# Performance work log

Hardware: AMD Instinct MI355X
Metric: run time of the kernel (lower is better)

The kernel has to match this reference:

```python
import jax, jax.numpy as jnp
import numpy as np

D_MODEL = 1024
D_MEMORY = 768
NUM_HEADS = 16
HEAD_DIM = D_MODEL // NUM_HEADS


def _linear_params(key, d_in, d_out):
    kw, kb = jax.random.split(key)
    bound = 1.0 / np.sqrt(d_in)
    W = jax.random.uniform(kw, (d_out, d_in), jnp.float32, -bound, bound)
    b = jax.random.uniform(kb, (d_out,), jnp.float32, -bound, bound)
    return W, b


def setup_inputs() -> dict:
    key = jax.random.key(0)
    ks = jax.random.split(key, 9)
    B, S, M = 2, 2048, 4096
    query = jax.random.normal(ks[0], (B, S, D_MODEL), jnp.float32)
    memory_keys = jax.random.normal(ks[1], (B, M, D_MEMORY), jnp.float32)
    memory_values = jax.random.normal(ks[2], (B, M, D_MEMORY), jnp.float32)
    Wq, bq = _linear_params(ks[3], D_MODEL, D_MODEL)
    Wk, bk = _linear_params(ks[4], D_MEMORY, D_MODEL)
    Wv, bv = _linear_params(ks[5], D_MEMORY, D_MODEL)
    Wo, bo = _linear_params(ks[6], D_MODEL, D_MODEL)
    Wg1, bg1 = _linear_params(ks[7], 2 * D_MODEL, D_MODEL)
    Wg2, bg2 = _linear_params(ks[8], D_MODEL, 1)
    return dict(query=query, memory_keys=memory_keys, memory_values=memory_values,
                Wq=Wq, bq=bq, Wk=Wk, bk=bk, Wv=Wv, bv=bv, Wo=Wo, bo=bo,
                Wg1=Wg1, bg1=bg1, Wg2=Wg2, bg2=bg2)


def reference(query, memory_keys, memory_values,
              Wq, bq, Wk, bk, Wv, bv, Wo, bo, Wg1, bg1, Wg2, bg2):
    B, S, _ = query.shape
    M = memory_keys.shape[1]
    H, Dh = NUM_HEADS, HEAD_DIM
    # projections (torch Linear: x @ W.T + b)
    Q = (query @ Wq.T + bq).reshape(B, S, H, Dh)
    K = (memory_keys @ Wk.T + bk).reshape(B, M, H, Dh)
    V = (memory_values @ Wv.T + bv).reshape(B, M, H, Dh)
    scale = Dh ** -0.5
    attn = jnp.einsum('bshd,bmhd->bhsm', Q, K) * scale
    attn = jax.nn.softmax(attn, axis=-1)
    retrieved = jnp.einsum('bhsm,bmhd->bshd', attn, V).reshape(B, S, H * Dh)
    retrieved = retrieved @ Wo.T + bo
    # gate: Linear -> SiLU -> Linear -> Sigmoid on [query; retrieved]
    g = jnp.concatenate([query, retrieved], axis=-1) @ Wg1.T + bg1
    g = jax.nn.silu(g)
    gate = jax.nn.sigmoid(g @ Wg2.T + bg2)  # [B,S,1]
    return query + gate * retrieved
```

## Files before the change

kernel.cpp:

```cpp
#include <hip/hip_runtime.h>

typedef __attribute__((ext_vector_type(8))) __bf16 bf16x8;
typedef __attribute__((ext_vector_type(4))) float f32x4;
typedef __attribute__((ext_vector_type(8))) unsigned short u16x8;

__device__ __forceinline__ ushort f2bf(float x) {
    unsigned u = __builtin_bit_cast(unsigned, x);
    unsigned r = u + 0x7fffu + ((u >> 16) & 1u);
    return (ushort)(r >> 16);
}
__device__ __forceinline__ float bf2f(ushort u) {
    unsigned v = ((unsigned)u) << 16;
    return __builtin_bit_cast(float, v);
}

__device__ __forceinline__ unsigned cvtpk(float lo, float hi) {
    unsigned r;
    asm("v_cvt_pk_bf16_f32 %0, %1, %2" : "=v"(r) : "v"(lo), "v"(hi));
    return r;
}

__device__ __forceinline__ void gload16(const void* g, void* l) {
    __builtin_amdgcn_global_load_lds(
        (const __attribute__((address_space(1))) void*)g,
        (__attribute__((address_space(3))) void*)l,
        16, 0, 0);
}

__global__ __launch_bounds__(256) void cvt_f32_bf16(const float* __restrict__ in,
                                                    ushort* __restrict__ out, int n4) {
    int i = blockIdx.x * 256 + threadIdx.x;
    int stride = gridDim.x * 256;
    for (; i < n4; i += stride) {
        float4 v = ((const float4*)in)[i];
        ushort4 o;
        o.x = f2bf(v.x); o.y = f2bf(v.y); o.z = f2bf(v.z); o.w = f2bf(v.w);
        ((ushort4*)out)[i] = o;
    }
}

__global__ __launch_bounds__(256) void cvt_query_cat(const float* __restrict__ in,
                                                     ushort* __restrict__ cat) {
    const int r = blockIdx.x, t = threadIdx.x;
    float4 v = ((const float4*)(in + (size_t)r * 1024))[t];
    ushort4 o;
    o.x = f2bf(v.x); o.y = f2bf(v.y); o.z = f2bf(v.z); o.w = f2bf(v.w);
    ((ushort4*)(cat + (size_t)r * 2048))[t] = o;
}

template<int EPI>
__global__ __launch_bounds__(256) void gemm_bt(
    const ushort* __restrict__ A, int lda,
    const ushort* __restrict__ Bw, int ldb,
    const float* __restrict__ bias,
    ushort* __restrict__ o_bf, int ld0,
    float* __restrict__ o_f32,
    int K, float scale)
{
    __shared__ __align__(1024) char smem[49152];
    char* As = smem;
    char* Bs = smem + 32768;
    const int t = threadIdx.x, w = t >> 6, l = t & 63, g = l >> 4, c = l & 15;
    const int wr = w >> 1, wc = w & 1;
    const long m0 = (long)blockIdx.y * 128, n0 = (long)blockIdx.x * 64;
    const size_t ldaB = (size_t)lda * 2, ldbB = (size_t)ldb * 2;
    const int swz = (c & 7) << 4;

    f32x4 acc[4][2];
#pragma unroll
    for (int i = 0; i < 4; ++i)
#pragma unroll
        for (int j = 0; j < 2; ++j) acc[i][j] = (f32x4)0.0f;

    auto stage = [&](int kt, int bufsel) {
        const char* Ab = (const char*)A + (size_t)kt * 128;
        const char* Bb = (const char*)Bw + (size_t)kt * 128;
#pragma unroll
        for (int i = 0; i < 4; ++i) {
            int o = (i * 4 + w) * 1024 + l * 16;
            int row = o >> 7, cb = o & 127;
            gload16(Ab + (size_t)(m0 + row) * ldaB + (cb ^ ((row & 7) << 4)),
                    As + bufsel * 16384 + (i * 4 + w) * 1024);
        }
#pragma unroll
        for (int i = 0; i < 2; ++i) {
            int o = (i * 4 + w) * 1024 + l * 16;
            int row = o >> 7, cb = o & 127;
            gload16(Bb + (size_t)(n0 + row) * ldbB + (cb ^ ((row & 7) << 4)),
                    Bs + bufsel * 8192 + (i * 4 + w) * 1024);
        }
    };

    const int nkt = K >> 6;
    stage(0, 0);
    __syncthreads();

    for (int kt = 0; kt < nkt; ++kt) {
        const int cur = kt & 1;
        if (kt + 1 < nkt) stage(kt + 1, cur ^ 1);
        const char* Ac = As + cur * 16384;
        const char* Bc = Bs + cur * 8192;
        bf16x8 af[2][4], bfr[2][2];
#pragma unroll
        for (int kf = 0; kf < 2; ++kf) {
            int cbk = (kf * 64 + g * 16) ^ swz;
#pragma unroll
            for (int i = 0; i < 4; ++i)
                af[kf][i] = *(const bf16x8*)(Ac + (wr * 64 + i * 16 + c) * 128 + cbk);
#pragma unroll
            for (int j = 0; j < 2; ++j)
                bfr[kf][j] = *(const bf16x8*)(Bc + (wc * 32 + j * 16 + c) * 128 + cbk);
        }
#pragma unroll
        for (int kf = 0; kf < 2; ++kf)
#pragma unroll
            for (int i = 0; i < 4; ++i)
#pragma unroll
                for (int j = 0; j < 2; ++j)
                    acc[i][j] = __builtin_amdgcn_mfma_f32_16x16x32_bf16(
                        af[kf][i], bfr[kf][j], acc[i][j], 0, 0, 0);
        __syncthreads();
    }

#pragma unroll
    for (int i = 0; i < 4; ++i)
#pragma unroll
        for (int j = 0; j < 2; ++j) {
            const long col = n0 + wc * 32 + j * 16 + c;
            const float bs = bias[col];
            const long rowb = m0 + wr * 64 + i * 16 + g * 4;
            if (EPI == 1) {
                ushort4 o;
                o.x = f2bf(acc[i][j][0] + bs);
                o.y = f2bf(acc[i][j][1] + bs);
                o.z = f2bf(acc[i][j][2] + bs);
                o.w = f2bf(acc[i][j][3] + bs);
                *(ushort4*)(o_bf + col * (long)ld0 + rowb) = o;
            } else {
#pragma unroll
                for (int jj = 0; jj < 4; ++jj) {
                    const long row = rowb + jj;
                    const float v = acc[i][j][jj] + bs;
                    if (EPI == 0) {
                        o_bf[row * (long)ld0 + col] = f2bf(v * scale);
                    } else if (EPI == 2) {
                        o_f32[row * (long)ld0 + col] = v;
                        o_bf[row * 2048 + col] = f2bf(v);
                    } else {
                        const float sv = v / (1.0f + __expf(-v));
                        o_bf[row * (long)ld0 + col] = f2bf(sv);
                    }
                }
            }
        }
}

__global__ __launch_bounds__(256, 4) void attn_fwd(
    const ushort* __restrict__ qp, const ushort* __restrict__ kp,
    const ushort* __restrict__ vT, ushort* __restrict__ out)
{
    __shared__ __align__(1024) char smem[40960];
    const int t = threadIdx.x, w = t >> 6, l = t & 63, g = l >> 4, c = l & 15;
    const int b = blockIdx.z, h = blockIdx.y;
    const int s0 = blockIdx.x * 64 + w * 16;
    const int swz = (c & 7) << 4;

    const size_t qbase = ((size_t)b * 2048 + s0 + c) * 1024 + h * 64 + g * 8;
    const bf16x8 qf0 = *(const bf16x8*)(qp + qbase);
    const bf16x8 qf1 = *(const bf16x8*)(qp + qbase + 32);

    const u16x8 ones_u = (u16x8)(ushort)0x3F80;
    const bf16x8 ones = __builtin_bit_cast(bf16x8, ones_u);

    f32x4 oacc[4];
    f32x4 lacc = (f32x4)0.0f;
#pragma unroll
    for (int d = 0; d < 4; ++d) oacc[d] = (f32x4)0.0f;
    float mrow = -1e30f;

    const char* kpB = (const char*)kp + (size_t)b * 4096 * 2048 + h * 128;
    const char* vTB = (const char*)vT + (size_t)h * 64 * 16384 + (size_t)b * 4096 * 2;
    char* Pw = smem + 32768 + w * 2048;

    auto stage = [&](int mt, int bufsel) {
#pragma unroll
        for (int i = 0; i < 2; ++i) {
            int o = (i * 4 + w) * 1024 + l * 16;
            int row = o >> 7, cb = o & 127;
            gload16(kpB + (size_t)(mt + row) * 2048 + (cb ^ ((row & 7) << 4)),
                    smem + bufsel * 8192 + (i * 4 + w) * 1024);
            gload16(vTB + (size_t)row * 16384 + (size_t)mt * 2 + (cb ^ ((row & 7) << 4)),
                    smem + 16384 + bufsel * 8192 + (i * 4 + w) * 1024);
        }
    };

    stage(0, 0);
    __syncthreads();

    for (int ti = 0; ti < 64; ++ti) {
        const int cur = ti & 1;
        if (ti < 63) stage((ti + 1) << 6, cur ^ 1);
        const char* Ksc = smem + cur * 8192;
        const char* Vsc = smem + 16384 + cur * 8192;

        f32x4 sacc[4];
#pragma unroll
        for (int mf = 0; mf < 4; ++mf) sacc[mf] = (f32x4)0.0f;
#pragma unroll
        for (int kf = 0; kf < 2; ++kf) {
            const int cbk = (kf * 64 + g * 16) ^ swz;
            const bf16x8 q = kf ? qf1 : qf0;
#pragma unroll
            for (int mf = 0; mf < 4; ++mf) {
                bf16x8 kb = *(const bf16x8*)(Ksc + (mf * 16 + c) * 128 + cbk);
                sacc[mf] = __builtin_amdgcn_mfma_f32_16x16x32_bf16(kb, q, sacc[mf], 0, 0, 0);
            }
        }

        float tm;
        {
            float a0 = fmaxf(fmaxf(sacc[0][0], sacc[0][1]), fmaxf(sacc[0][2], sacc[0][3]));
            float a1 = fmaxf(fmaxf(sacc[1][0], sacc[1][1]), fmaxf(sacc[1][2], sacc[1][3]));
            float a2 = fmaxf(fmaxf(sacc[2][0], sacc[2][1]), fmaxf(sacc[2][2], sacc[2][3]));
            float a3 = fmaxf(fmaxf(sacc[3][0], sacc[3][1]), fmaxf(sacc[3][2], sacc[3][3]));
            tm = fmaxf(fmaxf(a0, a1), fmaxf(a2, a3));
        }
        tm = fmaxf(tm, __shfl_xor(tm, 16));
        tm = fmaxf(tm, __shfl_xor(tm, 32));

        if (!__all(tm <= mrow + 8.0f)) {
            const float nm = fmaxf(mrow, tm);
            const float al = exp2f(mrow - nm);
            mrow = nm;
#pragma unroll
            for (int j = 0; j < 4; ++j) {
                const float alr = __shfl(al, g * 4 + j);
                lacc[j] *= alr;
#pragma unroll
                for (int df = 0; df < 4; ++df) oacc[df][j] *= alr;
            }
        }

        asm volatile("" ::: "memory");
#pragma unroll
        for (int mf = 0; mf < 4; ++mf) {
            const float p0 = exp2f(sacc[mf][0] - mrow);
            const float p1 = exp2f(sacc[mf][1] - mrow);
            const float p2 = exp2f(sacc[mf][2] - mrow);
            const float p3 = exp2f(sacc[mf][3] - mrow);
            const unsigned u0 = cvtpk(p0, p1);
            const unsigned u1 = cvtpk(p2, p3);
            const unsigned long long pw = ((unsigned long long)u1 << 32) | (unsigned long long)u0;
            *(unsigned long long*)(Pw + c * 128 + ((mf * 32 + g * 8) ^ swz)) = pw;
        }
        asm volatile("s_waitcnt lgkmcnt(0)" ::: "memory");
        __builtin_amdgcn_sched_barrier(0);
#pragma unroll
        for (int km = 0; km < 2; ++km) {
            const int cbm = (km * 64 + g * 16) ^ swz;
            const bf16x8 pa = *(const bf16x8*)(Pw + c * 128 + cbm);
            lacc = __builtin_amdgcn_mfma_f32_16x16x32_bf16(pa, ones, lacc, 0, 0, 0);
#pragma unroll
            for (int df = 0; df < 4; ++df) {
                bf16x8 vb = *(const bf16x8*)(Vsc + (df * 16 + c) * 128 + cbm);
                oacc[df] = __builtin_amdgcn_mfma_f32_16x16x32_bf16(pa, vb, oacc[df], 0, 0, 0);
            }
        }
        __builtin_amdgcn_sched_barrier(0);
        __syncthreads();
    }

    const size_t obase = ((size_t)b * 2048 + s0 + g * 4) * 1024 + h * 64 + c;
#pragma unroll
    for (int j = 0; j < 4; ++j) {
        const float rinv = 1.0f / lacc[j];
#pragma unroll
        for (int df = 0; df < 4; ++df)
            out[obase + (size_t)j * 1024 + df * 16] = f2bf(oacc[df][j] * rinv);
    }
}

__global__ __launch_bounds__(256) void gate_out_k(
    const ushort* __restrict__ gs, const float* __restrict__ Wg2,
    const float* __restrict__ bg2, const float* __restrict__ query,
    const float* __restrict__ retr, float* __restrict__ out)
{
    const int r = blockIdx.x, t = threadIdx.x, w = t >> 6, l = t & 63;
    ushort4 gv = ((const ushort4*)(gs + (size_t)r * 1024))[t];
    float4 wv = ((const float4*)Wg2)[t];
    float p = bf2f(gv.x) * wv.x + bf2f(gv.y) * wv.y + bf2f(gv.z) * wv.z + bf2f(gv.w) * wv.w;
    for (int m = 1; m < 64; m <<= 1) p += __shfl_xor(p, m);
    __shared__ float red[4];
    if (l == 0) red[w] = p;
    __syncthreads();
    const float dot = red[0] + red[1] + red[2] + red[3] + bg2[0];
    const float gate = 1.0f / (1.0f + __expf(-dot));
    float4 q = ((const float4*)(query + (size_t)r * 1024))[t];
    float4 rt = ((const float4*)(retr + (size_t)r * 1024))[t];
    float4 o;
    o.x = q.x + gate * rt.x; o.y = q.y + gate * rt.y;
    o.z = q.z + gate * rt.z; o.w = q.w + gate * rt.w;
    ((float4*)(out + (size_t)r * 1024))[t] = o;
}

extern "C" void kernel_launch(void* const* d_in, const int* in_sizes, int n_in,
                              void* d_out, int out_size, void* d_ws, size_t ws_size,
                              hipStream_t stream) {
    const float* query = (const float*)d_in[0];
    const float* mkeys = (const float*)d_in[1];
    const float* mvals = (const float*)d_in[2];
    const float* Wq  = (const float*)d_in[3];
    const float* bq  = (const float*)d_in[4];
    const float* Wk  = (const float*)d_in[5];
    const float* bk  = (const float*)d_in[6];
    const float* Wv  = (const float*)d_in[7];
    const float* bv  = (const float*)d_in[8];
    const float* Wo  = (const float*)d_in[9];
    const float* bo  = (const float*)d_in[10];
    const float* Wg1 = (const float*)d_in[11];
    const float* bg1 = (const float*)d_in[12];
    const float* Wg2 = (const float*)d_in[13];
    const float* bg2 = (const float*)d_in[14];
    float* outF = (float*)d_out;

    char* ws = (char*)d_ws;
    size_t off = 0;
    auto take = [&](size_t bytes) { char* p = ws + off; off += (bytes + 255) & ~(size_t)255; return p; };
    ushort* cat    = (ushort*)take((size_t)4096 * 2048 * 2);
    ushort* mkbf   = (ushort*)take((size_t)8192 * 768 * 2);
    ushort* mvbf   = (ushort*)take((size_t)8192 * 768 * 2);
    ushort* wqbf   = (ushort*)take((size_t)1024 * 1024 * 2);
    ushort* wkbf   = (ushort*)take((size_t)1024 * 768 * 2);
    ushort* wvbf   = (ushort*)take((size_t)1024 * 768 * 2);
    ushort* wobf   = (ushort*)take((size_t)1024 * 1024 * 2);
    ushort* wg1bf  = (ushort*)take((size_t)1024 * 2048 * 2);
    ushort* qproj  = (ushort*)take((size_t)4096 * 1024 * 2);
    ushort* kproj  = (ushort*)take((size_t)8192 * 1024 * 2);
    ushort* vprojT = (ushort*)take((size_t)1024 * 8192 * 2);
    ushort* attno  = (ushort*)take((size_t)4096 * 1024 * 2);
    float*  retro  = (float*)take((size_t)4096 * 1024 * 4);
    ushort* gsilu  = (ushort*)take((size_t)4096 * 1024 * 2);

    cvt_query_cat<<<4096, 256, 0, stream>>>(query, cat);
    cvt_f32_bf16<<<2048, 256, 0, stream>>>(mkeys, mkbf, 8192 * 768 / 4);
    cvt_f32_bf16<<<2048, 256, 0, stream>>>(mvals, mvbf, 8192 * 768 / 4);
    cvt_f32_bf16<<<512, 256, 0, stream>>>(Wq, wqbf, 1024 * 1024 / 4);
    cvt_f32_bf16<<<512, 256, 0, stream>>>(Wk, wkbf, 1024 * 768 / 4);
    cvt_f32_bf16<<<512, 256, 0, stream>>>(Wv, wvbf, 1024 * 768 / 4);
    cvt_f32_bf16<<<512, 256, 0, stream>>>(Wo, wobf, 1024 * 1024 / 4);
    cvt_f32_bf16<<<512, 256, 0, stream>>>(Wg1, wg1bf, 1024 * 2048 / 4);

    const float qscale = 0.125f * 1.44269504088896340736f;
    gemm_bt<0><<<dim3(16, 32), 256, 0, stream>>>(cat, 2048, wqbf, 1024, bq, qproj, 1024, nullptr, 1024, qscale);
    gemm_bt<0><<<dim3(16, 64), 256, 0, stream>>>(mkbf, 768, wkbf, 768, bk, kproj, 1024, nullptr, 768, 1.0f);
    gemm_bt<1><<<dim3(16, 64), 256, 0, stream>>>(mvbf, 768, wvbf, 768, bv, vprojT, 8192, nullptr, 768, 1.0f);
    attn_fwd<<<dim3(32, 16, 2), 256, 0, stream>>>(qproj, kproj, vprojT, attno);
    gemm_bt<2><<<dim3(16, 32), 256, 0, stream>>>(attno, 1024, wobf, 1024, bo, cat + 1024, 1024, retro, 1024, 1.0f);
    gemm_bt<3><<<dim3(16, 32), 256, 0, stream>>>(cat, 2048, wg1bf, 2048, bg1, gsilu, 1024, nullptr, 2048, 1.0f);
    gate_out_k<<<4096, 256, 0, stream>>>(gsilu, Wg2, bg2, query, retro, outF);
}
```

Before: 405.2 us.

## Triple-buffer GEMM and attention loads, double attention rows per wave, merge conversion kernels

The GEMM and attention kernels move from double to triple-buffered LDS staging. They replace __syncthreads with partial vmcnt waits plus s_barrier, so a tile can stay in flight while the current one is computed. Attention now processes 32 query rows per wave (two 16-row groups) sharing each K/V tile read, which halves the grid and the K/V traffic per query. The seven conversion launches are merged into two kernels. In exchange, the larger LDS footprint and higher register use lower occupancy, now declared as 2 blocks per CU.

```diff
diff --git a/kernel.cpp b/kernel.cpp
--- a/kernel.cpp
+++ b/kernel.cpp
@@ -27,16 +27,42 @@
         16, 0, 0);
 }
 
-__global__ __launch_bounds__(256) void cvt_f32_bf16(const float* __restrict__ in,
-                                                    ushort* __restrict__ out, int n4) {
-    int i = blockIdx.x * 256 + threadIdx.x;
-    int stride = gridDim.x * 256;
-    for (; i < n4; i += stride) {
-        float4 v = ((const float4*)in)[i];
-        ushort4 o;
-        o.x = f2bf(v.x); o.y = f2bf(v.y); o.z = f2bf(v.z); o.w = f2bf(v.w);
-        ((ushort4*)out)[i] = o;
-    }
+#define MFMA16(a, b, cIn) __builtin_amdgcn_mfma_f32_16x16x32_bf16((a), (b), (cIn), 0, 0, 0)
+
+__global__ __launch_bounds__(256) void cvt_kv(const float* __restrict__ a, ushort* __restrict__ ab,
+                                              const float* __restrict__ bsrc, ushort* __restrict__ bb,
+                                              int n4) {
+    const int stride = gridDim.x * 256;
+    for (int i = blockIdx.x * 256 + threadIdx.x; i < n4; i += stride) {
+        float4 v = ((const float4*)a)[i];
+        ushort4 o; o.x = f2bf(v.x); o.y = f2bf(v.y); o.z = f2bf(v.z); o.w = f2bf(v.w);
+        ((ushort4*)ab)[i] = o;
+    }
+    for (int i = blockIdx.x * 256 + threadIdx.x; i < n4; i += stride) {
+        float4 v = ((const float4*)bsrc)[i];
+        ushort4 o; o.x = f2bf(v.x); o.y = f2bf(v.y); o.z = f2bf(v.z); o.w = f2bf(v.w);
+        ((ushort4*)bb)[i] = o;
+    }
+}
+
+__global__ __launch_bounds__(256) void cvt_weights(
+    const float* __restrict__ s0, ushort* __restrict__ d0, int n0,
+    const float* __restrict__ s1, ushort* __restrict__ d1, int n1,
+    const float* __restrict__ s2, ushort* __restrict__ d2, int n2,
+    const float* __restrict__ s3, ushort* __restrict__ d3, int n3,
+    const float* __restrict__ s4, ushort* __restrict__ d4, int n4c) {
+    const int stride = gridDim.x * 256;
+    const int t0 = blockIdx.x * 256 + threadIdx.x;
+#define CVT_SEG(S, D, N)                                                  \
+    for (int i = t0; i < (N); i += stride) {                              \
+        float4 v = ((const float4*)(S))[i];                               \
+        ushort4 o; o.x = f2bf(v.x); o.y = f2bf(v.y);                      \
+        o.z = f2bf(v.z); o.w = f2bf(v.w);                                 \
+        ((ushort4*)(D))[i] = o;                                           \
+    }
+    CVT_SEG(s0, d0, n0) CVT_SEG(s1, d1, n1) CVT_SEG(s2, d2, n2)
+    CVT_SEG(s3, d3, n3) CVT_SEG(s4, d4, n4c)
+#undef CVT_SEG
 }
 
 __global__ __launch_bounds__(256) void cvt_query_cat(const float* __restrict__ in,
@@ -49,7 +75,7 @@
 }
 
 template<int EPI>
-__global__ __launch_bounds__(256) void gemm_bt(
+__global__ __launch_bounds__(256, 2) void gemm_bt(
     const ushort* __restrict__ A, int lda,
     const ushort* __restrict__ Bw, int ldb,
     const float* __restrict__ bias,
@@ -57,14 +83,29 @@
     float* __restrict__ o_f32,
     int K, float scale)
 {
-    __shared__ __align__(1024) char smem[49152];
-    char* As = smem;
-    char* Bs = smem + 32768;
+    __shared__ __align__(1024) char smem[73728];
     const int t = threadIdx.x, w = t >> 6, l = t & 63, g = l >> 4, c = l & 15;
     const int wr = w >> 1, wc = w & 1;
     const long m0 = (long)blockIdx.y * 128, n0 = (long)blockIdx.x * 64;
     const size_t ldaB = (size_t)lda * 2, ldbB = (size_t)ldb * 2;
     const int swz = (c & 7) << 4;
+    const int o0 = w * 1024 + l * 16;
+
+    auto gsrc = [&](const char* base, size_t ldB, long r0, int o) {
+        const int row = o >> 7, cb = o & 127;
+        return base + (size_t)(r0 + row) * ldB + (cb ^ ((row & 7) << 4));
+    };
+    const char* aP0 = gsrc((const char*)A, ldaB, m0, o0);
+    const char* aP1 = gsrc((const char*)A, ldaB, m0, o0 + 4096);
+    const char* aP2 = gsrc((const char*)A, ldaB, m0, o0 + 8192);
+    const char* aP3 = gsrc((const char*)A, ldaB, m0, o0 + 12288);
+    const char* bP0 = gsrc((const char*)Bw, ldbB, n0, o0);
+    const char* bP1 = gsrc((const char*)Bw, ldbB, n0, o0 + 4096);
+
+    const int aRd0 = (wr * 64 + c) * 128 + ((g * 16) ^ swz);
+    const int aRd1 = aRd0 ^ 64;
+    const int bRd0 = (wc * 32 + c) * 128 + ((g * 16) ^ swz);
+    const int bRd1 = bRd0 ^ 64;
 
     f32x4 acc[4][2];
 #pragma unroll
@@ -72,54 +113,54 @@
 #pragma unroll
         for (int j = 0; j < 2; ++j) acc[i][j] = (f32x4)0.0f;
 
-    auto stage = [&](int kt, int bufsel) {
-        const char* Ab = (const char*)A + (size_t)kt * 128;
-        const char* Bb = (const char*)Bw + (size_t)kt * 128;
-#pragma unroll
-        for (int i = 0; i < 4; ++i) {
-            int o = (i * 4 + w) * 1024 + l * 16;
-            int row = o >> 7, cb = o & 127;
-            gload16(Ab + (size_t)(m0 + row) * ldaB + (cb ^ ((row & 7) << 4)),
-                    As + bufsel * 16384 + (i * 4 + w) * 1024);
-        }
-#pragma unroll
-        for (int i = 0; i < 2; ++i) {
-            int o = (i * 4 + w) * 1024 + l * 16;
-            int row = o >> 7, cb = o & 127;
-            gload16(Bb + (size_t)(n0 + row) * ldbB + (cb ^ ((row & 7) << 4)),
-                    Bs + bufsel * 8192 + (i * 4 + w) * 1024);
-        }
+    auto stage = [&](int slotA) {
+        gload16(aP0, smem + slotA + w * 1024);
+        gload16(aP1, smem + slotA + 4096 + w * 1024);
+        gload16(aP2, smem + slotA + 8192 + w * 1024);
+        gload16(aP3, smem + slotA + 12288 + w * 1024);
+        gload16(bP0, smem + 49152 + (slotA >> 1) + w * 1024);
+        gload16(bP1, smem + 49152 + (slotA >> 1) + 4096 + w * 1024);
+        aP0 += 128; aP1 += 128; aP2 += 128; aP3 += 128;
+        bP0 += 128; bP1 += 128;
     };
 
     const int nkt = K >> 6;
-    stage(0, 0);
-    __syncthreads();
-
+    stage(0);
+    stage(16384);
+    asm volatile("s_waitcnt vmcnt(6)" ::: "memory");
+    __builtin_amdgcn_s_barrier();
+
+    int rdA = 0, stA = 32768;
     for (int kt = 0; kt < nkt; ++kt) {
-        const int cur = kt & 1;
-        if (kt + 1 < nkt) stage(kt + 1, cur ^ 1);
-        const char* Ac = As + cur * 16384;
-        const char* Bc = Bs + cur * 8192;
-        bf16x8 af[2][4], bfr[2][2];
+        const bool pf = (kt + 2 < nkt);
+        if (pf) {
+            stage(stA);
+            stA = (stA == 32768) ? 0 : stA + 16384;
+        }
+        const char* Ac = smem + rdA;
+        const char* Bc = smem + 49152 + (rdA >> 1);
 #pragma unroll
         for (int kf = 0; kf < 2; ++kf) {
-            int cbk = (kf * 64 + g * 16) ^ swz;
-#pragma unroll
-            for (int i = 0; i < 4; ++i)
-                af[kf][i] = *(const bf16x8*)(Ac + (wr * 64 + i * 16 + c) * 128 + cbk);
-#pragma unroll
-            for (int j = 0; j < 2; ++j)
-                bfr[kf][j] = *(const bf16x8*)(Bc + (wc * 32 + j * 16 + c) * 128 + cbk);
-        }
-#pragma unroll
-        for (int kf = 0; kf < 2; ++kf)
-#pragma unroll
-            for (int i = 0; i < 4; ++i)
-#pragma unroll
-                for (int j = 0; j < 2; ++j)
-                    acc[i][j] = __builtin_amdgcn_mfma_f32_16x16x32_bf16(
-                        af[kf][i], bfr[kf][j], acc[i][j], 0, 0, 0);
-        __syncthreads();
+            const int ar = kf ? aRd1 : aRd0, br = kf ? bRd1 : bRd0;
+            bf16x8 af0 = *(const bf16x8*)(Ac + 0 + ar);
+            bf16x8 af1 = *(const bf16x8*)(Ac + 2048 + ar);
+            bf16x8 af2 = *(const bf16x8*)(Ac + 4096 + ar);
+            bf16x8 af3 = *(const bf16x8*)(Ac + 6144 + ar);
+            bf16x8 bf0 = *(const bf16x8*)(Bc + 0 + br);
+            bf16x8 bf1 = *(const bf16x8*)(Bc + 2048 + br);
+            acc[0][0] = MFMA16(af0, bf0, acc[0][0]);
+            acc[0][1] = MFMA16(af0, bf1, acc[0][1]);
+            acc[1][0] = MFMA16(af1, bf0, acc[1][0]);
+            acc[1][1] = MFMA16(af1, bf1, acc[1][1]);
+            acc[2][0] = MFMA16(af2, bf0, acc[2][0]);
+            acc[2][1] = MFMA16(af2, bf1, acc[2][1]);
+            acc[3][0] = MFMA16(af3, bf0, acc[3][0]);
+            acc[3][1] = MFMA16(af3, bf1, acc[3][1]);
+        }
+        rdA = (rdA == 32768) ? 0 : rdA + 16384;
+        if (pf) asm volatile("s_waitcnt vmcnt(6)" ::: "memory");
+        else    asm volatile("s_waitcnt vmcnt(0)" ::: "memory");
+        __builtin_amdgcn_s_barrier();
     }
 
 #pragma unroll
@@ -155,128 +196,188 @@
         }
 }
 
-__global__ __launch_bounds__(256, 4) void attn_fwd(
+__global__ __launch_bounds__(256, 2) void attn_fwd(
     const ushort* __restrict__ qp, const ushort* __restrict__ kp,
     const ushort* __restrict__ vT, ushort* __restrict__ out)
 {
-    __shared__ __align__(1024) char smem[40960];
+    __shared__ __align__(1024) char smem[65536];
     const int t = threadIdx.x, w = t >> 6, l = t & 63, g = l >> 4, c = l & 15;
     const int b = blockIdx.z, h = blockIdx.y;
-    const int s0 = blockIdx.x * 64 + w * 16;
+    const int s0 = blockIdx.x * 128 + w * 32;
     const int swz = (c & 7) << 4;
 
-    const size_t qbase = ((size_t)b * 2048 + s0 + c) * 1024 + h * 64 + g * 8;
-    const bf16x8 qf0 = *(const bf16x8*)(qp + qbase);
-    const bf16x8 qf1 = *(const bf16x8*)(qp + qbase + 32);
+    const size_t qbaseA = ((size_t)b * 2048 + s0 + c) * 1024 + h * 64 + g * 8;
+    const bf16x8 qA0 = *(const bf16x8*)(qp + qbaseA);
+    const bf16x8 qA1 = *(const bf16x8*)(qp + qbaseA + 32);
+    const bf16x8 qB0 = *(const bf16x8*)(qp + qbaseA + 16 * 1024);
+    const bf16x8 qB1 = *(const bf16x8*)(qp + qbaseA + 16 * 1024 + 32);
 
     const u16x8 ones_u = (u16x8)(ushort)0x3F80;
     const bf16x8 ones = __builtin_bit_cast(bf16x8, ones_u);
 
-    f32x4 oacc[4];
-    f32x4 lacc = (f32x4)0.0f;
-#pragma unroll
-    for (int d = 0; d < 4; ++d) oacc[d] = (f32x4)0.0f;
-    float mrow = -1e30f;
+    f32x4 oaccA[4], oaccB[4];
+    f32x4 laccA = (f32x4)0.0f, laccB = (f32x4)0.0f;
+#pragma unroll
+    for (int d = 0; d < 4; ++d) { oaccA[d] = (f32x4)0.0f; oaccB[d] = (f32x4)0.0f; }
+    float mrowA = -1e30f, mrowB = -1e30f;
+
+    const int kb0 = c * 128 + ((g * 16) ^ swz);
+    const int kb1 = kb0 ^ 64;
+    const int Pbase = 49152 + w * 4096;
+    const int pw0 = Pbase + c * 128 + ((g * 8) ^ swz);
+    const int pr0 = Pbase + kb0;
+    const int pr1 = pr0 ^ 64;
 
     const char* kpB = (const char*)kp + (size_t)b * 4096 * 2048 + h * 128;
     const char* vTB = (const char*)vT + (size_t)h * 64 * 16384 + (size_t)b * 4096 * 2;
-    char* Pw = smem + 32768 + w * 2048;
-
-    auto stage = [&](int mt, int bufsel) {
-#pragma unroll
-        for (int i = 0; i < 2; ++i) {
-            int o = (i * 4 + w) * 1024 + l * 16;
-            int row = o >> 7, cb = o & 127;
-            gload16(kpB + (size_t)(mt + row) * 2048 + (cb ^ ((row & 7) << 4)),
-                    smem + bufsel * 8192 + (i * 4 + w) * 1024);
-            gload16(vTB + (size_t)row * 16384 + (size_t)mt * 2 + (cb ^ ((row & 7) << 4)),
-                    smem + 16384 + bufsel * 8192 + (i * 4 + w) * 1024);
-        }
+    const int o0 = w * 1024 + l * 16;
+    auto mksrc = [&](const char* base, size_t ldB, int o) {
+        const int row = o >> 7, cb = o & 127;
+        return base + (size_t)row * ldB + (cb ^ ((row & 7) << 4));
     };
-
-    stage(0, 0);
-    __syncthreads();
-
+    const char* kg0 = mksrc(kpB, 2048, o0);
+    const char* kg1 = mksrc(kpB, 2048, o0 + 4096);
+    const char* vg0 = mksrc(vTB, 16384, o0);
+    const char* vg1 = mksrc(vTB, 16384, o0 + 4096);
+
+    auto stage = [&](int stK) {
+        gload16(kg0, smem + stK + w * 1024);
+        gload16(kg1, smem + stK + 4096 + w * 1024);
+        gload16(vg0, smem + 24576 + stK + w * 1024);
+        gload16(vg1, smem + 24576 + stK + 4096 + w * 1024);
+        kg0 += 131072; kg1 += 131072; vg0 += 128; vg1 += 128;
+    };
+
+    stage(0);
+    stage(8192);
+    asm volatile("s_waitcnt vmcnt(4)" ::: "memory");
+    __builtin_amdgcn_s_barrier();
+
+    int rdK = 0, stK = 16384;
     for (int ti = 0; ti < 64; ++ti) {
-        const int cur = ti & 1;
-        if (ti < 63) stage((ti + 1) << 6, cur ^ 1);
-        const char* Ksc = smem + cur * 8192;
-        const char* Vsc = smem + 16384 + cur * 8192;
-
-        f32x4 sacc[4];
-#pragma unroll
-        for (int mf = 0; mf < 4; ++mf) sacc[mf] = (f32x4)0.0f;
+        const bool pf = (ti < 62);
+        if (pf) {
+            stage(stK);
+            stK = (stK == 16384) ? 0 : stK + 8192;
+        }
+        const char* Ksc = smem + rdK;
+        const char* Vsc = smem + 24576 + rdK;
+
+        f32x4 sA[4], sB[4];
+#pragma unroll
+        for (int mf = 0; mf < 4; ++mf) { sA[mf] = (f32x4)0.0f; sB[mf] = (f32x4)0.0f; }
 #pragma unroll
         for (int kf = 0; kf < 2; ++kf) {
-            const int cbk = (kf * 64 + g * 16) ^ swz;
-            const bf16x8 q = kf ? qf1 : qf0;
+            const int kbase = kf ? kb1 : kb0;
+            const bf16x8 qa = kf ? qA1 : qA0;
+            const bf16x8 qb = kf ? qB1 : qB0;
 #pragma unroll
             for (int mf = 0; mf < 4; ++mf) {
-                bf16x8 kb = *(const bf16x8*)(Ksc + (mf * 16 + c) * 128 + cbk);
-                sacc[mf] = __builtin_amdgcn_mfma_f32_16x16x32_bf16(kb, q, sacc[mf], 0, 0, 0);
-            }
-        }
-
-        float tm;
+                const bf16x8 kb = *(const bf16x8*)(Ksc + mf * 2048 + kbase);
+                sA[mf] = MFMA16(kb, qa, sA[mf]);
+                sB[mf] = MFMA16(kb, qb, sB[mf]);
+            }
+        }
+
+        float tmA;
         {
-            float a0 = fmaxf(fmaxf(sacc[0][0], sacc[0][1]), fmaxf(sacc[0][2], sacc[0][3]));
-            float a1 = fmaxf(fmaxf(sacc[1][0], sacc[1][1]), fmaxf(sacc[1][2], sacc[1][3]));
-            float a2 = fmaxf(fmaxf(sacc[2][0], sacc[2][1]), fmaxf(sacc[2][2], sacc[2][3]));
-            float a3 = fmaxf(fmaxf(sacc[3][0], sacc[3][1]), fmaxf(sacc[3][2], sacc[3][3]));
-            tm = fmaxf(fmaxf(a0, a1), fmaxf(a2, a3));
-        }
-        tm = fmaxf(tm, __shfl_xor(tm, 16));
-        tm = fmaxf(tm, __shfl_xor(tm, 32));
-
-        if (!__all(tm <= mrow + 8.0f)) {
-            const float nm = fmaxf(mrow, tm);
-            const float al = exp2f(mrow - nm);
-            mrow = nm;
+            float a0 = fmaxf(fmaxf(sA[0][0], sA[0][1]), fmaxf(sA[0][2], sA[0][3]));
+            float a1 = fmaxf(fmaxf(sA[1][0], sA[1][1]), fmaxf(sA[1][2], sA[1][3]));
+            float a2 = fmaxf(fmaxf(sA[2][0], sA[2][1]), fmaxf(sA[2][2], sA[2][3]));
+            float a3 = fmaxf(fmaxf(sA[3][0], sA[3][1]), fmaxf(sA[3][2], sA[3][3]));
+            tmA = fmaxf(fmaxf(a0, a1), fmaxf(a2, a3));
+        }
+        tmA = fmaxf(tmA, __shfl_xor(tmA, 16));
+        tmA = fmaxf(tmA, __shfl_xor(tmA, 32));
+        if (!__all(tmA <= mrowA + 8.0f)) {
+            const float nm = fmaxf(mrowA, tmA);
+            const float al = exp2f(mrowA - nm);
+            mrowA = nm;
 #pragma unroll
             for (int j = 0; j < 4; ++j) {
                 const float alr = __shfl(al, g * 4 + j);
-                lacc[j] *= alr;
-#pragma unroll
-                for (int df = 0; df < 4; ++df) oacc[df][j] *= alr;
+                laccA[j] *= alr;
+                oaccA[0][j] *= alr; oaccA[1][j] *= alr;
+                oaccA[2][j] *= alr; oaccA[3][j] *= alr;
+            }
+        }
+        float tmB;
+        {
+            float a0 = fmaxf(fmaxf(sB[0][0], sB[0][1]), fmaxf(sB[0][2], sB[0][3]));
+            float a1 = fmaxf(fmaxf(sB[1][0], sB[1][1]), fmaxf(sB[1][2], sB[1][3]));
+            float a2 = fmaxf(fmaxf(sB[2][0], sB[2][1]), fmaxf(sB[2][2], sB[2][3]));
+            float a3 = fmaxf(fmaxf(sB[3][0], sB[3][1]), fmaxf(sB[3][2], sB[3][3]));
+            tmB = fmaxf(fmaxf(a0, a1), fmaxf(a2, a3));
+        }
+        tmB = fmaxf(tmB, __shfl_xor(tmB, 16));
+        tmB = fmaxf(tmB, __shfl_xor(tmB, 32));
+        if (!__all(tmB <= mrowB + 8.0f)) {
+            const float nm = fmaxf(mrowB, tmB);
+            const float al = exp2f(mrowB - nm);
+            mrowB = nm;
+#pragma unroll
+            for (int j = 0; j < 4; ++j) {
+                const float alr = __shfl(al, g * 4 + j);
+                laccB[j] *= alr;
+                oaccB[0][j] *= alr; oaccB[1][j] *= alr;
+                oaccB[2][j] *= alr; oaccB[3][j] *= alr;
             }
         }
 
         asm volatile("" ::: "memory");
 #pragma unroll
         for (int mf = 0; mf < 4; ++mf) {
-            const float p0 = exp2f(sacc[mf][0] - mrow);
-            const float p1 = exp2f(sacc[mf][1] - mrow);
-            const float p2 = exp2f(sacc[mf][2] - mrow);
-            const float p3 = exp2f(sacc[mf][3] - mrow);
-            const unsigned u0 = cvtpk(p0, p1);
-            const unsigned u1 = cvtpk(p2, p3);
-            const unsigned long long pw = ((unsigned long long)u1 << 32) | (unsigned long long)u0;
-            *(unsigned long long*)(Pw + c * 128 + ((mf * 32 + g * 8) ^ swz)) = pw;
+            {
+                const float p0 = exp2f(sA[mf][0] - mrowA);
+                const float p1 = exp2f(sA[mf][1] - mrowA);
+                const float p2 = exp2f(sA[mf][2] - mrowA);
+                const float p3 = exp2f(sA[mf][3] - mrowA);
+                *(unsigned long long*)(smem + (pw0 ^ (mf * 32))) =
+                    ((unsigned long long)cvtpk(p2, p3) << 32) | cvtpk(p0, p1);
+            }
+            {
+                const float p0 = exp2f(sB[mf][0] - mrowB);
+                const float p1 = exp2f(sB[mf][1] - mrowB);
+                const float p2 = exp2f(sB[mf][2] - mrowB);
+                const float p3 = exp2f(sB[mf][3] - mrowB);
+                *(unsigned long long*)(smem + 2048 + (pw0 ^ (mf * 32))) =
+                    ((unsigned long long)cvtpk(p2, p3) << 32) | cvtpk(p0, p1);
+            }
         }
         asm volatile("s_waitcnt lgkmcnt(0)" ::: "memory");
         __builtin_amdgcn_sched_barrier(0);
 #pragma unroll
         for (int km = 0; km < 2; ++km) {
-            const int cbm = (km * 64 + g * 16) ^ swz;
-            const bf16x8 pa = *(const bf16x8*)(Pw + c * 128 + cbm);
-            lacc = __builtin_amdgcn_mfma_f32_16x16x32_bf16(pa, ones, lacc, 0, 0, 0);
+            const int prk = km ? pr1 : pr0;
+            const int vbase = km ? kb1 : kb0;
+            const bf16x8 paA = *(const bf16x8*)(smem + prk);
+            const bf16x8 paB = *(const bf16x8*)(smem + 2048 + prk);
+            laccA = MFMA16(paA, ones, laccA);
+            laccB = MFMA16(paB, ones, laccB);
 #pragma unroll
             for (int df = 0; df < 4; ++df) {
-                bf16x8 vb = *(const bf16x8*)(Vsc + (df * 16 + c) * 128 + cbm);
-                oacc[df] = __builtin_amdgcn_mfma_f32_16x16x32_bf16(pa, vb, oacc[df], 0, 0, 0);
+                const bf16x8 vb = *(const bf16x8*)(Vsc + df * 2048 + vbase);
+                oaccA[df] = MFMA16(paA, vb, oaccA[df]);
+                oaccB[df] = MFMA16(paB, vb, oaccB[df]);
             }
         }
         __builtin_amdgcn_sched_barrier(0);
-        __syncthreads();
+        rdK = (rdK == 16384) ? 0 : rdK + 8192;
+        if (pf) asm volatile("s_waitcnt vmcnt(4)" ::: "memory");
+        else    asm volatile("s_waitcnt vmcnt(0)" ::: "memory");
+        __builtin_amdgcn_s_barrier();
     }
 
     const size_t obase = ((size_t)b * 2048 + s0 + g * 4) * 1024 + h * 64 + c;
 #pragma unroll
     for (int j = 0; j < 4; ++j) {
-        const float rinv = 1.0f / lacc[j];
-#pragma unroll
-        for (int df = 0; df < 4; ++df)
-            out[obase + (size_t)j * 1024 + df * 16] = f2bf(oacc[df][j] * rinv);
+        const float rinvA = 1.0f / laccA[j];
+        const float rinvB = 1.0f / laccB[j];
+#pragma unroll
+        for (int df = 0; df < 4; ++df) {
+            out[obase + (size_t)j * 1024 + df * 16] = f2bf(oaccA[df][j] * rinvA);
+            out[obase + (size_t)(j + 16) * 1024 + df * 16] = f2bf(oaccB[df][j] * rinvB);
+        }
     }
 }
 
@@ -342,19 +443,18 @@
     ushort* gsilu  = (ushort*)take((size_t)4096 * 1024 * 2);
 
     cvt_query_cat<<<4096, 256, 0, stream>>>(query, cat);
-    cvt_f32_bf16<<<2048, 256, 0, stream>>>(mkeys, mkbf, 8192 * 768 / 4);
-    cvt_f32_bf16<<<2048, 256, 0, stream>>>(mvals, mvbf, 8192 * 768 / 4);
-    cvt_f32_bf16<<<512, 256, 0, stream>>>(Wq, wqbf, 1024 * 1024 / 4);
-    cvt_f32_bf16<<<512, 256, 0, stream>>>(Wk, wkbf, 1024 * 768 / 4);
-    cvt_f32_bf16<<<512, 256, 0, stream>>>(Wv, wvbf, 1024 * 768 / 4);
-    cvt_f32_bf16<<<512, 256, 0, stream>>>(Wo, wobf, 1024 * 1024 / 4);
-    cvt_f32_bf16<<<512, 256, 0, stream>>>(Wg1, wg1bf, 1024 * 2048 / 4);
+    cvt_kv<<<2048, 256, 0, stream>>>(mkeys, mkbf, mvals, mvbf, 8192 * 768 / 4);
+    cvt_weights<<<1024, 256, 0, stream>>>(Wq, wqbf, 1024 * 1024 / 4,
+                                          Wk, wkbf, 1024 * 768 / 4,
+                                          Wv, wvbf, 1024 * 768 / 4,
+                                          Wo, wobf, 1024 * 1024 / 4,
+                                          Wg1, wg1bf, 1024 * 2048 / 4);
 
     const float qscale = 0.125f * 1.44269504088896340736f;
     gemm_bt<0><<<dim3(16, 32), 256, 0, stream>>>(cat, 2048, wqbf, 1024, bq, qproj, 1024, nullptr, 1024, qscale);
     gemm_bt<0><<<dim3(16, 64), 256, 0, stream>>>(mkbf, 768, wkbf, 768, bk, kproj, 1024, nullptr, 768, 1.0f);
     gemm_bt<1><<<dim3(16, 64), 256, 0, stream>>>(mvbf, 768, wvbf, 768, bv, vprojT, 8192, nullptr, 768, 1.0f);
-    attn_fwd<<<dim3(32, 16, 2), 256, 0, stream>>>(qproj, kproj, vprojT, attno);
+    attn_fwd<<<dim3(16, 16, 2), 256, 0, stream>>>(qproj, kproj, vprojT, attno);
     gemm_bt<2><<<dim3(16, 32), 256, 0, stream>>>(attno, 1024, wobf, 1024, bo, cat + 1024, 1024, retro, 1024, 1.0f);
     gemm_bt<3><<<dim3(16, 32), 256, 0, stream>>>(cat, 2048, wg1bf, 2048, bg1, gsilu, 1024, nullptr, 2048, 1.0f);
     gate_out_k<<<4096, 256, 0, stream>>>(gsilu, Wg2, bg2, query, retro, outF);
```

Result: no change. 398.0 us (-1.8%).
